# Kernel tuning notes

Measured on AMD Instinct MI355X. Metric: run time of the kernel, lower is better.

The kernel has to match this reference:

```python
import jax, jax.numpy as jnp
import numpy as np

N_NODES = 100000
D_FEAT = 128
K_NEIGH = 16
N_LAYERS = 2
F_OUT = 128  # features = [128, 128]


def setup_inputs() -> dict:
    key = jax.random.key(0)
    k1, k2, k3 = jax.random.split(key, 3)
    feats = jax.random.normal(k1, (N_NODES, D_FEAT), dtype=jnp.float32)
    # per-layer sampled neighbor indices (fresh sampling each layer, as in the source)
    neigh_idx = jax.random.randint(k2, (N_LAYERS, N_NODES, K_NEIGH), 0, N_NODES, dtype=jnp.int32)
    # Dense kernels: input is concat(self, mean_neighbors) -> 2*D; both layers 256 -> 128
    Ws = jax.random.normal(k3, (N_LAYERS, 2 * D_FEAT, F_OUT), dtype=jnp.float32) * (1.0 / np.sqrt(2 * D_FEAT))
    bs = jnp.zeros((N_LAYERS, F_OUT), dtype=jnp.float32)
    return {"feats": feats, "neigh_idx": neigh_idx, "Ws": Ws, "bs": bs}


def reference(feats, neigh_idx, Ws, bs):
    """GraphSAGE (mean aggregator): per layer, gather sampled neighbors,
    mean-aggregate, concat with self, Dense; relu between layers.
    Returns the last-layer Dense output (pre-relu), matching `new_feats`
    returned by the source module.
    """
    h = feats  # [N, D]
    z = h
    for l in range(Ws.shape[0]):
        neigh = h[neigh_idx[l]]              # [N, K, D] irregular gather
        agg = neigh.mean(axis=1)             # [N, D] mean aggregation
        cat = jnp.concatenate([h, agg], axis=-1)  # [N, 2D]
        z = cat @ Ws[l] + bs[l]              # [N, F]
        h = jax.nn.relu(z)
    return z
```

## Files before the change

kernel.cpp:

```cpp
#include <hip/hip_runtime.h>

#define N_NODES 100000
#define D 128
#define K 16
#define CATK 256
#define MB 32
#define PAD 8
#define LDSW (CATK + PAD)
#define ZW 132

typedef __attribute__((ext_vector_type(8))) short bf16x8;
typedef __attribute__((ext_vector_type(4))) float f32x4;
typedef __attribute__((ext_vector_type(2))) float f32x2;

__device__ __forceinline__ unsigned short f2bf(float f) {
    union { float f; unsigned u; } v; v.f = f;
    unsigned u = v.u;
    return (unsigned short)((u + 0x7fffu + ((u >> 16) & 1u)) >> 16);
}

__device__ __forceinline__ unsigned pk4(float a, float b, float c, float d) {
    int w = __builtin_amdgcn_cvt_pk_fp8_f32(a, b, 0, false);
    w = __builtin_amdgcn_cvt_pk_fp8_f32(c, d, w, true);
    return (unsigned)w;
}

__device__ __forceinline__ void dec4(unsigned w, float* acc) {
    f32x2 lo = __builtin_amdgcn_cvt_pk_f32_fp8((int)w, false);
    f32x2 hi = __builtin_amdgcn_cvt_pk_f32_fp8((int)w, true);
    acc[0] += lo.x; acc[1] += lo.y; acc[2] += hi.x; acc[3] += hi.y;
}

__global__ void cvt_all(const float* __restrict__ feats, const float* __restrict__ Ws,
                        unsigned* __restrict__ f8, unsigned short* __restrict__ Wt) {
    int tid = blockIdx.x * 256 + threadIdx.x;
    int i = tid * 16;
    if (i < N_NODES * D) {
        const float4* p = (const float4*)(feats + i);
        float4 v0 = p[0], v1 = p[1], v2 = p[2], v3 = p[3];
        uint4 o;
        o.x = pk4(v0.x, v0.y, v0.z, v0.w);
        o.y = pk4(v1.x, v1.y, v1.z, v1.w);
        o.z = pk4(v2.x, v2.y, v2.z, v2.w);
        o.w = pk4(v3.x, v3.y, v3.z, v3.w);
        *(uint4*)(f8 + i / 4) = o;
    }
    if (tid < 2 * CATK * D) {
        int l = tid / (CATK * D);
        int r = tid % (CATK * D);
        int n = r / CATK, k = r % CATK;
        Wt[tid] = f2bf(Ws[l * CATK * D + k * D + n]);
    }
}

template <int LAYER>
__launch_bounds__(256)
__global__ void sage_layer(const float* __restrict__ self_f32,
                           const unsigned short* __restrict__ self_bf,
                           const unsigned char* __restrict__ g8,
                           const int* __restrict__ idx,
                           const unsigned short* __restrict__ Wt,
                           const float* __restrict__ bias,
                           unsigned short* __restrict__ h_out,
                           unsigned char* __restrict__ h8_out,
                           float* __restrict__ z_out) {
    __shared__ __align__(16) char smraw[MB * LDSW * 2];
    unsigned short (*cat)[LDSW] = (unsigned short (*)[LDSW])smraw;
    float (*zb)[ZW] = (float (*)[ZW])smraw;
    __shared__ int sIdx[MB][K];

    const int t = threadIdx.x;
    const int base = blockIdx.x * MB;
    const int lane = t & 63;
    const int wave = t >> 6;
    const int q = lane >> 4;
    const int nlo = lane & 15;

    if (t < MB * K / 4)
        ((int4*)&sIdx[0][0])[t] = ((const int4*)(idx + base * K))[t];
    __syncthreads();

    {
        const int m = t >> 3;
        const int c = (t & 7) * 16;
        const int node = base + m;

        if (LAYER == 0) {
            const float4* sp = (const float4*)(self_f32 + (size_t)node * D + c);
            float sv[16];
            *(f32x4*)&sv[0]  = *(const f32x4*)&sp[0];
            *(f32x4*)&sv[4]  = *(const f32x4*)&sp[1];
            *(f32x4*)&sv[8]  = *(const f32x4*)&sp[2];
            *(f32x4*)&sv[12] = *(const f32x4*)&sp[3];
            unsigned w[8];
#pragma unroll
            for (int j = 0; j < 8; ++j)
                w[j] = (unsigned)f2bf(sv[2 * j]) | ((unsigned)f2bf(sv[2 * j + 1]) << 16);
            *(uint4*)&cat[m][c]     = make_uint4(w[0], w[1], w[2], w[3]);
            *(uint4*)&cat[m][c + 8] = make_uint4(w[4], w[5], w[6], w[7]);
        } else {
            const uint4* sp = (const uint4*)(self_bf + (size_t)node * D + c);
            *(uint4*)&cat[m][c]     = sp[0];
            *(uint4*)&cat[m][c + 8] = sp[1];
        }

        float acc[16];
#pragma unroll
        for (int i = 0; i < 16; ++i) acc[i] = 0.f;
#pragma unroll 4
        for (int k = 0; k < K; ++k) {
            uint4 u = *(const uint4*)(g8 + (size_t)sIdx[m][k] * D + c);
            dec4(u.x, acc + 0);
            dec4(u.y, acc + 4);
            dec4(u.z, acc + 8);
            dec4(u.w, acc + 12);
        }
        unsigned pk[8];
#pragma unroll
        for (int j = 0; j < 8; ++j) {
            unsigned short a = f2bf(acc[2 * j] * (1.f / 16.f));
            unsigned short b = f2bf(acc[2 * j + 1] * (1.f / 16.f));
            pk[j] = (unsigned)a | ((unsigned)b << 16);
        }
        *(uint4*)&cat[m][D + c]     = make_uint4(pk[0], pk[1], pk[2], pk[3]);
        *(uint4*)&cat[m][D + c + 8] = make_uint4(pk[4], pk[5], pk[6], pk[7]);
    }

    bf16x8 bfrag[2][8];
#pragma unroll
    for (int ct = 0; ct < 2; ++ct) {
        int n = wave * 32 + ct * 16 + nlo;
        const unsigned short* wp = Wt + n * CATK + q * 8;
#pragma unroll
        for (int ks = 0; ks < 8; ++ks)
            bfrag[ct][ks] = *(const bf16x8*)(wp + ks * 32);
    }

    __syncthreads();

    f32x4 acc00 = {}, acc01 = {}, acc10 = {}, acc11 = {};
#pragma unroll
    for (int ks = 0; ks < 8; ++ks) {
        bf16x8 a0 = *(const bf16x8*)&cat[nlo][ks * 32 + q * 8];
        bf16x8 a1 = *(const bf16x8*)&cat[16 + nlo][ks * 32 + q * 8];
        acc00 = __builtin_amdgcn_mfma_f32_16x16x32_bf16(a0, bfrag[0][ks], acc00, 0, 0, 0);
        acc01 = __builtin_amdgcn_mfma_f32_16x16x32_bf16(a0, bfrag[1][ks], acc01, 0, 0, 0);
        acc10 = __builtin_amdgcn_mfma_f32_16x16x32_bf16(a1, bfrag[0][ks], acc10, 0, 0, 0);
        acc11 = __builtin_amdgcn_mfma_f32_16x16x32_bf16(a1, bfrag[1][ks], acc11, 0, 0, 0);
    }

    __syncthreads();
#pragma unroll
    for (int ct = 0; ct < 2; ++ct) {
        int col = wave * 32 + ct * 16 + nlo;
        float bv = bias[col];
        f32x4 v0 = (ct == 0) ? acc00 : acc01;
        f32x4 v1 = (ct == 0) ? acc10 : acc11;
#pragma unroll
        for (int r = 0; r < 4; ++r) {
            zb[q * 4 + r][col]      = v0[r] + bv;
            zb[16 + q * 4 + r][col] = v1[r] + bv;
        }
    }
    __syncthreads();
    {
        const int m = t >> 3;
        const int c = (t & 7) * 16;
        float x[16];
        *(f32x4*)&x[0]  = *(const f32x4*)&zb[m][c];
        *(f32x4*)&x[4]  = *(const f32x4*)&zb[m][c + 4];
        *(f32x4*)&x[8]  = *(const f32x4*)&zb[m][c + 8];
        *(f32x4*)&x[12] = *(const f32x4*)&zb[m][c + 12];
        size_t go = (size_t)(base + m) * D + c;
        if (LAYER == 1) {
            float4* zp = (float4*)(z_out + go);
            zp[0] = make_float4(x[0], x[1], x[2], x[3]);
            zp[1] = make_float4(x[4], x[5], x[6], x[7]);
            zp[2] = make_float4(x[8], x[9], x[10], x[11]);
            zp[3] = make_float4(x[12], x[13], x[14], x[15]);
        } else {
#pragma unroll
            for (int i = 0; i < 16; ++i) x[i] = x[i] > 0.f ? x[i] : 0.f;
            unsigned wb[8];
#pragma unroll
            for (int j = 0; j < 8; ++j)
                wb[j] = (unsigned)f2bf(x[2 * j]) | ((unsigned)f2bf(x[2 * j + 1]) << 16);
            uint4* hp = (uint4*)(h_out + go);
            hp[0] = make_uint4(wb[0], wb[1], wb[2], wb[3]);
            hp[1] = make_uint4(wb[4], wb[5], wb[6], wb[7]);
            uint4 o8;
            o8.x = pk4(x[0], x[1], x[2], x[3]);
            o8.y = pk4(x[4], x[5], x[6], x[7]);
            o8.z = pk4(x[8], x[9], x[10], x[11]);
            o8.w = pk4(x[12], x[13], x[14], x[15]);
            *(uint4*)(h8_out + go) = o8;
        }
    }
}

extern "C" void kernel_launch(void* const* d_in, const int* in_sizes, int n_in,
                              void* d_out, int out_size, void* d_ws, size_t ws_size,
                              hipStream_t stream) {
    const float* feats = (const float*)d_in[0];
    const int* neigh   = (const int*)d_in[1];
    const float* Ws    = (const float*)d_in[2];
    const float* bs    = (const float*)d_in[3];
    float* out = (float*)d_out;

    char* ws = (char*)d_ws;
    unsigned short* h1_bf  = (unsigned short*)(ws);
    unsigned char*  feats8 = (unsigned char*)(ws + 25600000);
    unsigned char*  h18    = (unsigned char*)(ws + 38400000);
    unsigned short* Wt     = (unsigned short*)(ws + 51200000);

    cvt_all<<<3125, 256, 0, stream>>>(feats, Ws, (unsigned*)feats8, Wt);

    sage_layer<0><<<N_NODES / MB, 256, 0, stream>>>(
        feats, nullptr, feats8, neigh, Wt, bs, h1_bf, h18, nullptr);
    sage_layer<1><<<N_NODES / MB, 256, 0, stream>>>(
        nullptr, h1_bf, h18, neigh + N_NODES * K, Wt + CATK * D, bs + D,
        nullptr, nullptr, out);
}
```

Before: 213.3 us.

## Fold neighbor mean into FP8 MFMA over gathered rows via async LDS loads

Rather than decoding and summing the 16 FP8 neighbor rows in VALU, the kernel loads them straight into LDS with global_load_lds. It then treats the neighbor sum as a GEMM reduction, running FP8 MFMA against a pre-scaled FP8 copy of the aggregate half of W and rescaling by 1/256 afterwards. The block now covers 16 nodes instead of 32, and launch bounds request 4 blocks per CU for more parallel gathers. The trade is 16x more MFMA work on the aggregate path and lower weight precision (FP8) for that half, in exchange for removing VALU decode/accumulate and register pressure.

```diff
diff --git a/kernel.cpp b/kernel.cpp
--- a/kernel.cpp
+++ b/kernel.cpp
@@ -3,36 +3,28 @@
 #define N_NODES 100000
 #define D 128
 #define K 16
-#define CATK 256
-#define MB 32
-#define PAD 8
-#define LDSW (CATK + PAD)
-#define ZW 132
+#define MB 16
 
 typedef __attribute__((ext_vector_type(8))) short bf16x8;
 typedef __attribute__((ext_vector_type(4))) float f32x4;
 typedef __attribute__((ext_vector_type(2))) float f32x2;
+
+#define LDS_BYTES 38208
 
 __device__ __forceinline__ unsigned short f2bf(float f) {
     union { float f; unsigned u; } v; v.f = f;
     unsigned u = v.u;
     return (unsigned short)((u + 0x7fffu + ((u >> 16) & 1u)) >> 16);
 }
-
 __device__ __forceinline__ unsigned pk4(float a, float b, float c, float d) {
     int w = __builtin_amdgcn_cvt_pk_fp8_f32(a, b, 0, false);
     w = __builtin_amdgcn_cvt_pk_fp8_f32(c, d, w, true);
     return (unsigned)w;
 }
 
-__device__ __forceinline__ void dec4(unsigned w, float* acc) {
-    f32x2 lo = __builtin_amdgcn_cvt_pk_f32_fp8((int)w, false);
-    f32x2 hi = __builtin_amdgcn_cvt_pk_f32_fp8((int)w, true);
-    acc[0] += lo.x; acc[1] += lo.y; acc[2] += hi.x; acc[3] += hi.y;
-}
-
 __global__ void cvt_all(const float* __restrict__ feats, const float* __restrict__ Ws,
-                        unsigned* __restrict__ f8, unsigned short* __restrict__ Wt) {
+                        unsigned* __restrict__ f8, unsigned short* __restrict__ Wt,
+                        unsigned char* __restrict__ W8) {
     int tid = blockIdx.x * 256 + threadIdx.x;
     int i = tid * 16;
     if (i < N_NODES * D) {
@@ -45,29 +37,32 @@
         o.w = pk4(v3.x, v3.y, v3.z, v3.w);
         *(uint4*)(f8 + i / 4) = o;
     }
-    if (tid < 2 * CATK * D) {
-        int l = tid / (CATK * D);
-        int r = tid % (CATK * D);
-        int n = r / CATK, k = r % CATK;
-        Wt[tid] = f2bf(Ws[l * CATK * D + k * D + n]);
+    if (tid < 2 * D * D) {
+        int l = tid >> 14, r = tid & 16383;
+        int n = r >> 7, k = r & 127;
+        const float* Wl = Ws + l * (2 * D * D);
+        Wt[tid] = f2bf(Wl[k * D + n]);
+        int w = __builtin_amdgcn_cvt_pk_fp8_f32(Wl[(D + k) * D + n] * 16.f, 0.f, 0, false);
+        W8[tid] = (unsigned char)(w & 0xff);
     }
 }
 
 template <int LAYER>
-__launch_bounds__(256)
+__launch_bounds__(256, 4)
 __global__ void sage_layer(const float* __restrict__ self_f32,
                            const unsigned short* __restrict__ self_bf,
                            const unsigned char* __restrict__ g8,
                            const int* __restrict__ idx,
                            const unsigned short* __restrict__ Wt,
+                           const unsigned char* __restrict__ W8,
                            const float* __restrict__ bias,
                            unsigned short* __restrict__ h_out,
                            unsigned char* __restrict__ h8_out,
                            float* __restrict__ z_out) {
-    __shared__ __align__(16) char smraw[MB * LDSW * 2];
-    unsigned short (*cat)[LDSW] = (unsigned short (*)[LDSW])smraw;
-    float (*zb)[ZW] = (float (*)[ZW])smraw;
-    __shared__ int sIdx[MB][K];
+    __shared__ __align__(16) char sm[LDS_BYTES];
+    unsigned short (*sSelf)[136] = (unsigned short (*)[136])(sm + 32768);
+    int (*sIdx)[17] = (int (*)[17])(sm + 37120);
+    float (*zb)[132] = (float (*)[132])sm;
 
     const int t = threadIdx.x;
     const int base = blockIdx.x * MB;
@@ -76,124 +71,104 @@
     const int q = lane >> 4;
     const int nlo = lane & 15;
 
-    if (t < MB * K / 4)
-        ((int4*)&sIdx[0][0])[t] = ((const int4*)(idx + base * K))[t];
+    sIdx[t >> 4][t & 15] = idx[(size_t)base * K + t];
+
+    {
+        int m = t >> 4, c = (t & 15) * 8;
+        if (LAYER == 0) {
+            const float4* sp = (const float4*)(self_f32 + (size_t)(base + m) * D + c);
+            float4 a = sp[0], b = sp[1];
+            unsigned w0 = (unsigned)f2bf(a.x) | ((unsigned)f2bf(a.y) << 16);
+            unsigned w1 = (unsigned)f2bf(a.z) | ((unsigned)f2bf(a.w) << 16);
+            unsigned w2 = (unsigned)f2bf(b.x) | ((unsigned)f2bf(b.y) << 16);
+            unsigned w3 = (unsigned)f2bf(b.z) | ((unsigned)f2bf(b.w) << 16);
+            *(uint4*)&sSelf[m][c] = make_uint4(w0, w1, w2, w3);
+        } else {
+            *(uint4*)&sSelf[m][c] = *(const uint4*)(self_bf + (size_t)(base + m) * D + c);
+        }
+    }
     __syncthreads();
 
-    {
-        const int m = t >> 3;
-        const int c = (t & 7) * 16;
-        const int node = base + m;
-
-        if (LAYER == 0) {
-            const float4* sp = (const float4*)(self_f32 + (size_t)node * D + c);
-            float sv[16];
-            *(f32x4*)&sv[0]  = *(const f32x4*)&sp[0];
-            *(f32x4*)&sv[4]  = *(const f32x4*)&sp[1];
-            *(f32x4*)&sv[8]  = *(const f32x4*)&sp[2];
-            *(f32x4*)&sv[12] = *(const f32x4*)&sp[3];
-            unsigned w[8];
 #pragma unroll
-            for (int j = 0; j < 8; ++j)
-                w[j] = (unsigned)f2bf(sv[2 * j]) | ((unsigned)f2bf(sv[2 * j + 1]) << 16);
-            *(uint4*)&cat[m][c]     = make_uint4(w[0], w[1], w[2], w[3]);
-            *(uint4*)&cat[m][c + 8] = make_uint4(w[4], w[5], w[6], w[7]);
-        } else {
-            const uint4* sp = (const uint4*)(self_bf + (size_t)node * D + c);
-            *(uint4*)&cat[m][c]     = sp[0];
-            *(uint4*)&cat[m][c + 8] = sp[1];
+    for (int nn = 0; nn < 4; ++nn) {
+        int n = wave * 4 + nn;
+#pragma unroll
+        for (int j = 0; j < 2; ++j) {
+            int m = j * 8 + (lane >> 3);
+            int node = sIdx[m][n];
+            int c = (((lane & 7) - m) << 4) & 127;
+            const void* gp = (const void*)(g8 + ((size_t)node << 7) + c);
+            void* lp = (void*)(sm + n * 2048 + j * 1024);
+            __builtin_amdgcn_global_load_lds(
+                (const __attribute__((address_space(1))) unsigned int*)gp,
+                (__attribute__((address_space(3))) unsigned int*)lp, 16, 0, 0);
         }
-
-        float acc[16];
-#pragma unroll
-        for (int i = 0; i < 16; ++i) acc[i] = 0.f;
-#pragma unroll 4
-        for (int k = 0; k < K; ++k) {
-            uint4 u = *(const uint4*)(g8 + (size_t)sIdx[m][k] * D + c);
-            dec4(u.x, acc + 0);
-            dec4(u.y, acc + 4);
-            dec4(u.z, acc + 8);
-            dec4(u.w, acc + 12);
-        }
-        unsigned pk[8];
-#pragma unroll
-        for (int j = 0; j < 8; ++j) {
-            unsigned short a = f2bf(acc[2 * j] * (1.f / 16.f));
-            unsigned short b = f2bf(acc[2 * j + 1] * (1.f / 16.f));
-            pk[j] = (unsigned)a | ((unsigned)b << 16);
-        }
-        *(uint4*)&cat[m][D + c]     = make_uint4(pk[0], pk[1], pk[2], pk[3]);
-        *(uint4*)&cat[m][D + c + 8] = make_uint4(pk[4], pk[5], pk[6], pk[7]);
     }
 
-    bf16x8 bfrag[2][8];
+    long b8[2][4];
+    bf16x8 bsf[2][4];
 #pragma unroll
-    for (int ct = 0; ct < 2; ++ct) {
-        int n = wave * 32 + ct * 16 + nlo;
-        const unsigned short* wp = Wt + n * CATK + q * 8;
+    for (int nt = 0; nt < 2; ++nt) {
+        int col = wave * 32 + nt * 16 + nlo;
 #pragma unroll
-        for (int ks = 0; ks < 8; ++ks)
-            bfrag[ct][ks] = *(const bf16x8*)(wp + ks * 32);
+        for (int ksm = 0; ksm < 4; ++ksm) {
+            b8[nt][ksm] = *(const long*)(W8 + (size_t)col * 128 + ksm * 32 + q * 8);
+            bsf[nt][ksm] = *(const bf16x8*)(Wt + (size_t)col * 128 + ksm * 32 + q * 8);
+        }
     }
 
     __syncthreads();
 
-    f32x4 acc00 = {}, acc01 = {}, acc10 = {}, acc11 = {};
+    f32x4 aAgg0 = {}, aAgg1 = {}, aSelf0 = {}, aSelf1 = {};
+#pragma unroll 8
+    for (int ks = 0; ks < 64; ++ks) {
+        int n = ks >> 2, ksm = ks & 3;
+        int ro = (ksm * 32 + q * 8 + nlo * 16) & 127;
+        long av = *(const long*)(sm + n * 2048 + nlo * 128 + ro);
+        aAgg0 = __builtin_amdgcn_mfma_f32_16x16x32_fp8_fp8(av, b8[0][ksm], aAgg0, 0, 0, 0);
+        aAgg1 = __builtin_amdgcn_mfma_f32_16x16x32_fp8_fp8(av, b8[1][ksm], aAgg1, 0, 0, 0);
+    }
 #pragma unroll
-    for (int ks = 0; ks < 8; ++ks) {
-        bf16x8 a0 = *(const bf16x8*)&cat[nlo][ks * 32 + q * 8];
-        bf16x8 a1 = *(const bf16x8*)&cat[16 + nlo][ks * 32 + q * 8];
-        acc00 = __builtin_amdgcn_mfma_f32_16x16x32_bf16(a0, bfrag[0][ks], acc00, 0, 0, 0);
-        acc01 = __builtin_amdgcn_mfma_f32_16x16x32_bf16(a0, bfrag[1][ks], acc01, 0, 0, 0);
-        acc10 = __builtin_amdgcn_mfma_f32_16x16x32_bf16(a1, bfrag[0][ks], acc10, 0, 0, 0);
-        acc11 = __builtin_amdgcn_mfma_f32_16x16x32_bf16(a1, bfrag[1][ks], acc11, 0, 0, 0);
+    for (int ks = 0; ks < 4; ++ks) {
+        bf16x8 av = *(const bf16x8*)&sSelf[nlo][ks * 32 + q * 8];
+        aSelf0 = __builtin_amdgcn_mfma_f32_16x16x32_bf16(av, bsf[0][ks], aSelf0, 0, 0, 0);
+        aSelf1 = __builtin_amdgcn_mfma_f32_16x16x32_bf16(av, bsf[1][ks], aSelf1, 0, 0, 0);
     }
 
     __syncthreads();
 #pragma unroll
-    for (int ct = 0; ct < 2; ++ct) {
-        int col = wave * 32 + ct * 16 + nlo;
+    for (int nt = 0; nt < 2; ++nt) {
+        int col = wave * 32 + nt * 16 + nlo;
         float bv = bias[col];
-        f32x4 v0 = (ct == 0) ? acc00 : acc01;
-        f32x4 v1 = (ct == 0) ? acc10 : acc11;
+        f32x4 vs = nt ? aSelf1 : aSelf0;
+        f32x4 va = nt ? aAgg1 : aAgg0;
 #pragma unroll
-        for (int r = 0; r < 4; ++r) {
-            zb[q * 4 + r][col]      = v0[r] + bv;
-            zb[16 + q * 4 + r][col] = v1[r] + bv;
-        }
+        for (int r = 0; r < 4; ++r)
+            zb[q * 4 + r][col] = vs[r] + va[r] * (1.0f / 256.0f) + bv;
     }
     __syncthreads();
     {
-        const int m = t >> 3;
-        const int c = (t & 7) * 16;
-        float x[16];
-        *(f32x4*)&x[0]  = *(const f32x4*)&zb[m][c];
-        *(f32x4*)&x[4]  = *(const f32x4*)&zb[m][c + 4];
-        *(f32x4*)&x[8]  = *(const f32x4*)&zb[m][c + 8];
-        *(f32x4*)&x[12] = *(const f32x4*)&zb[m][c + 12];
+        int m = t >> 4, c = (t & 15) * 8;
+        float x[8];
+        *(f32x4*)&x[0] = *(const f32x4*)&zb[m][c];
+        *(f32x4*)&x[4] = *(const f32x4*)&zb[m][c + 4];
         size_t go = (size_t)(base + m) * D + c;
         if (LAYER == 1) {
             float4* zp = (float4*)(z_out + go);
             zp[0] = make_float4(x[0], x[1], x[2], x[3]);
             zp[1] = make_float4(x[4], x[5], x[6], x[7]);
-            zp[2] = make_float4(x[8], x[9], x[10], x[11]);
-            zp[3] = make_float4(x[12], x[13], x[14], x[15]);
         } else {
 #pragma unroll
-            for (int i = 0; i < 16; ++i) x[i] = x[i] > 0.f ? x[i] : 0.f;
-            unsigned wb[8];
-#pragma unroll
-            for (int j = 0; j < 8; ++j)
-                wb[j] = (unsigned)f2bf(x[2 * j]) | ((unsigned)f2bf(x[2 * j + 1]) << 16);
-            uint4* hp = (uint4*)(h_out + go);
-            hp[0] = make_uint4(wb[0], wb[1], wb[2], wb[3]);
-            hp[1] = make_uint4(wb[4], wb[5], wb[6], wb[7]);
-            uint4 o8;
+            for (int i = 0; i < 8; ++i) x[i] = x[i] > 0.f ? x[i] : 0.f;
+            unsigned w0 = (unsigned)f2bf(x[0]) | ((unsigned)f2bf(x[1]) << 16);
+            unsigned w1 = (unsigned)f2bf(x[2]) | ((unsigned)f2bf(x[3]) << 16);
+            unsigned w2 = (unsigned)f2bf(x[4]) | ((unsigned)f2bf(x[5]) << 16);
+            unsigned w3 = (unsigned)f2bf(x[6]) | ((unsigned)f2bf(x[7]) << 16);
+            *(uint4*)(h_out + go) = make_uint4(w0, w1, w2, w3);
+            uint2 o8;
             o8.x = pk4(x[0], x[1], x[2], x[3]);
             o8.y = pk4(x[4], x[5], x[6], x[7]);
-            o8.z = pk4(x[8], x[9], x[10], x[11]);
-            o8.w = pk4(x[12], x[13], x[14], x[15]);
-            *(uint4*)(h8_out + go) = o8;
+            *(uint2*)(h8_out + go) = o8;
         }
     }
 }
@@ -212,12 +187,13 @@
     unsigned char*  feats8 = (unsigned char*)(ws + 25600000);
     unsigned char*  h18    = (unsigned char*)(ws + 38400000);
     unsigned short* Wt     = (unsigned short*)(ws + 51200000);
+    unsigned char*  W8     = (unsigned char*)(ws + 51265536);
 
-    cvt_all<<<3125, 256, 0, stream>>>(feats, Ws, (unsigned*)feats8, Wt);
+    cvt_all<<<3125, 256, 0, stream>>>(feats, Ws, (unsigned*)feats8, Wt, W8);
 
     sage_layer<0><<<N_NODES / MB, 256, 0, stream>>>(
-        feats, nullptr, feats8, neigh, Wt, bs, h1_bf, h18, nullptr);
+        feats, nullptr, feats8, neigh, Wt, W8, bs, h1_bf, h18, nullptr);
     sage_layer<1><<<N_NODES / MB, 256, 0, stream>>>(
-        nullptr, h1_bf, h18, neigh + N_NODES * K, Wt + CATK * D, bs + D,
+        nullptr, h1_bf, h18, neigh + N_NODES * K, Wt + D * D, W8 + D * D, bs + D,
         nullptr, nullptr, out);
 }
```

After: 237.0 us. +11.1%, slower.
